# Performance work log

Hardware: AMD Instinct MI355X
Metric: run time of the kernel (lower is better)

## Reference

```python
import jax, jax.numpy as jnp
import numpy as np

N = 100000
E = 1600000
D = 64
BETA = 1.0


def setup_inputs() -> dict:
    key = jax.random.key(0)
    ks = jax.random.split(key, 6)
    x = jax.random.normal(ks[0], (N, D), dtype=jnp.float32)
    edge_index = jax.random.randint(ks[1], (2, E), 0, N, dtype=jnp.int64)
    s = 1.0 / np.sqrt(D)
    Wm = jax.random.uniform(ks[2], (D, D), jnp.float32, -s, s)
    bm = jax.random.uniform(ks[3], (D,), jnp.float32, -s, s)
    Wr = jax.random.uniform(ks[4], (D, D), jnp.float32, -s, s)
    br = jax.random.uniform(ks[5], (D,), jnp.float32, -s, s)
    return {"x": x, "edge_index": edge_index, "Wm": Wm, "bm": bm, "Wr": Wr, "br": br}


def reference(x, edge_index, Wm, bm, Wr, br):
    row, col = edge_index[0], edge_index[1]
    # gather source features and apply message linear: [E, D]
    messages = x[row] @ Wm + bm
    scores = BETA * messages.mean(axis=-1)  # [E]
    # edge softmax over incoming edges of each destination node (col)
    seg_max = jax.ops.segment_max(scores, col, num_segments=N)  # [N]
    ex = jnp.exp(scores - seg_max[col])  # [E]
    seg_sum = jax.ops.segment_sum(ex, col, num_segments=N)  # [N]
    weights = ex / seg_sum[col]  # [E]
    # weighted scatter-add back to destinations
    out = jax.ops.segment_sum(messages * weights[:, None], col, num_segments=N)
    return out + (x @ Wr + br)
```

## Files before the change

### kernel.cpp

```cpp
#include <hip/hip_runtime.h>
#include <math.h>

#define N_NODES 100000
#define DIM 64
#define N_EDGES 1600000

#define NBF 782
#define BK_NODES 128
#define CAP 3072

#define SC_CHUNK 8192
#define SC_BLOCKS ((N_EDGES + SC_CHUNK - 1) / SC_CHUNK)

#define GEMM_BLOCKS ((N_NODES / 16 + 15) / 16)
#define PH_BLOCKS (SC_BLOCKS + GEMM_BLOCKS)

typedef _Float16 half8 __attribute__((ext_vector_type(8)));
typedef _Float16 half4 __attribute__((ext_vector_type(4)));
typedef float f32x4 __attribute__((ext_vector_type(4)));

__global__ __launch_bounds__(1024) void k_phase(
        const float* __restrict__ x,
        const float* __restrict__ Wm, const float* __restrict__ bm,
        const float* __restrict__ Wr, const float* __restrict__ br,
        const int* __restrict__ row, const int* __restrict__ col,
        int* __restrict__ cursor, unsigned int* __restrict__ pairs,
        _Float16* __restrict__ Mh, float* __restrict__ es,
        float* __restrict__ out) {
    __shared__ int cnt[NBF];
    __shared__ int base_l[NBF];
    __shared__ int base_g[NBF];
    __shared__ int wsum[16];
    __shared__ unsigned int stage[SC_CHUNK];
    __shared__ unsigned short stage_bk[SC_CHUNK];

    const int t = threadIdx.x;
    const int lane = t & 63;
    const int wid = t >> 6;

    if (blockIdx.x < SC_BLOCKS) {
        const int start = blockIdx.x * SC_CHUNK;
        const int mEnd = min(N_EDGES, start + SC_CHUNK);

        for (int i = t; i < NBF; i += 1024) cnt[i] = 0;
        __syncthreads();

        int rr[8], cc[8], lr[8];
#pragma unroll
        for (int k = 0; k < 8; ++k) {
            const int idx = start + k * 1024 + t;
            if (idx < mEnd) {
                cc[k] = col[idx];
                rr[k] = row[idx];
                lr[k] = atomicAdd(&cnt[cc[k] >> 7], 1);
            }
        }
        __syncthreads();

        const int v = (t < NBF) ? cnt[t] : 0;
        int inc = v;
#pragma unroll
        for (int o = 1; o < 64; o <<= 1) {
            const int u = __shfl_up(inc, o, 64);
            if (lane >= o) inc += u;
        }
        if (lane == 63) wsum[wid] = inc;
        __syncthreads();
        if (wid == 0) {
            const int wv = (lane < 16) ? wsum[lane] : 0;
            int winc = wv;
#pragma unroll
            for (int o = 1; o < 16; o <<= 1) {
                const int u = __shfl_up(winc, o, 64);
                if (lane >= o) winc += u;
            }
            if (lane < 16) wsum[lane] = winc - wv;
        }
        __syncthreads();
        if (t < NBF) {
            base_l[t] = inc - v + wsum[wid];
            if (v > 0) base_g[t] = atomicAdd(&cursor[t], v);
        }
        __syncthreads();

#pragma unroll
        for (int k = 0; k < 8; ++k) {
            const int idx = start + k * 1024 + t;
            if (idx < mEnd) {
                const int bk = cc[k] >> 7;
                const int slot = base_l[bk] + lr[k];
                stage[slot] = ((unsigned int)rr[k] << 7) | (unsigned int)(cc[k] & 127);
                stage_bk[slot] = (unsigned short)bk;
            }
        }
        __syncthreads();

        const int m = mEnd - start;
        for (int i = t; i < m; i += 1024) {
            const int bk = stage_bk[i];
            const int gslot = base_g[bk] + (i - base_l[bk]);
            if (gslot < CAP) pairs[(size_t)bk * CAP + gslot] = stage[i];
        }
        return;
    }

    const int wave = (blockIdx.x - SC_BLOCKS) * 16 + wid;
    if (wave >= N_NODES / 16) return;
    const int quad = lane >> 4;
    const int l15 = lane & 15;
    const int row0 = wave * 16;

    half8 bfrag[8][2];
#pragma unroll
    for (int ct = 0; ct < 8; ++ct) {
        const float* W = (ct < 4) ? Wm : Wr;
        const int c = (ct & 3) * 16 + l15;
#pragma unroll
        for (int kc = 0; kc < 2; ++kc) {
            half8 f;
#pragma unroll
            for (int j = 0; j < 8; ++j)
                f[j] = (_Float16)W[(kc * 32 + quad * 8 + j) * DIM + c];
            bfrag[ct][kc] = f;
        }
    }

    half8 afrag[2];
#pragma unroll
    for (int kc = 0; kc < 2; ++kc) {
        const float* xp = x + (size_t)(row0 + l15) * DIM + kc * 32 + quad * 8;
        const float4 x0 = *(const float4*)xp;
        const float4 x1 = *(const float4*)(xp + 4);
        half8 f;
        f[0] = (_Float16)x0.x; f[1] = (_Float16)x0.y;
        f[2] = (_Float16)x0.z; f[3] = (_Float16)x0.w;
        f[4] = (_Float16)x1.x; f[5] = (_Float16)x1.y;
        f[6] = (_Float16)x1.z; f[7] = (_Float16)x1.w;
        afrag[kc] = f;
    }

    f32x4 acc[8];
#pragma unroll
    for (int ct = 0; ct < 8; ++ct) {
        f32x4 a = {0.f, 0.f, 0.f, 0.f};
        a = __builtin_amdgcn_mfma_f32_16x16x32_f16(afrag[0], bfrag[ct][0], a, 0, 0, 0);
        a = __builtin_amdgcn_mfma_f32_16x16x32_f16(afrag[1], bfrag[ct][1], a, 0, 0, 0);
        acc[ct] = a;
    }

    float rsum[4] = {0.f, 0.f, 0.f, 0.f};
#pragma unroll
    for (int ct = 0; ct < 8; ++ct) {
        const float bias = (ct < 4) ? bm[(ct & 3) * 16 + l15]
                                    : br[(ct & 3) * 16 + l15];
#pragma unroll
        for (int r = 0; r < 4; ++r) {
            const float v = acc[ct][r] + bias;
            const size_t idx = (size_t)(row0 + quad * 4 + r) * DIM + (ct & 3) * 16 + l15;
            if (ct < 4) {
                Mh[idx] = (_Float16)v;
                rsum[r] += v;
            } else {
                out[idx] = v;
            }
        }
    }
#pragma unroll
    for (int o = 1; o <= 8; o <<= 1) {
#pragma unroll
        for (int r = 0; r < 4; ++r) rsum[r] += __shfl_xor(rsum[r], o, 64);
    }
    if (l15 == 0) {
#pragma unroll
        for (int r = 0; r < 4; ++r)
            es[row0 + quad * 4 + r] = __expf(rsum[r] * (1.0f / DIM));
    }
}

__global__ __launch_bounds__(512) void k_bucket_gather(
        const unsigned int* __restrict__ pairs, const int* __restrict__ cursor,
        const float* __restrict__ es, const half4* __restrict__ Mh4,
        float4* __restrict__ out4) {
    __shared__ unsigned int sorted[CAP];
    __shared__ int cnt[BK_NODES];
    __shared__ int off[BK_NODES];
    const int b = blockIdx.x;
    const int t = threadIdx.x;
    const int m = min(cursor[b], CAP);
    const size_t base = (size_t)b * CAP;

    if (t < BK_NODES) cnt[t] = 0;
    __syncthreads();

    unsigned int pk[6];
    int rk[6];
#pragma unroll
    for (int k = 0; k < 6; ++k) {
        const int i = k * 512 + t;
        if (i < m) {
            pk[k] = pairs[base + i];
            rk[k] = atomicAdd(&cnt[pk[k] & 127u], 1);
        }
    }
    __syncthreads();

    int v = 0;
    if (t < BK_NODES) {
        v = cnt[t];
        off[t] = v;
    }
    __syncthreads();
    for (int o = 1; o < BK_NODES; o <<= 1) {
        int add = 0;
        if (t < BK_NODES && t >= o) add = off[t - o];
        __syncthreads();
        if (t < BK_NODES) off[t] += add;
        __syncthreads();
    }
    if (t < BK_NODES) off[t] -= v;
    __syncthreads();

#pragma unroll
    for (int k = 0; k < 6; ++k) {
        const int i = k * 512 + t;
        if (i < m) sorted[off[pk[k] & 127u] + rk[k]] = pk[k];
    }
    __syncthreads();

    const int g = t >> 4;
    const int gl = t & 15;
    for (int c = g; c < BK_NODES; c += 32) {
        const int node = b * BK_NODES + c;
        if (node >= N_NODES) break;
        const int s0i = off[c];
        const int len = cnt[c];
        if (len == 0) continue;

        float a0x = 0.f, a0y = 0.f, a0z = 0.f, a0w = 0.f, l0 = 0.f;
        float a1x = 0.f, a1y = 0.f, a1z = 0.f, a1w = 0.f, l1 = 0.f;
        int j = 0;
        for (; j + 1 < len; j += 2) {
            const int s0 = (int)(sorted[s0i + j] >> 7);
            const int s1 = (int)(sorted[s0i + j + 1] >> 7);
            const float w0 = es[s0];
            const float w1 = es[s1];
            const half4 m0 = Mh4[(size_t)s0 * 16 + gl];
            const half4 m1 = Mh4[(size_t)s1 * 16 + gl];
            l0 += w0; l1 += w1;
            a0x = fmaf(w0, (float)m0[0], a0x); a0y = fmaf(w0, (float)m0[1], a0y);
            a0z = fmaf(w0, (float)m0[2], a0z); a0w = fmaf(w0, (float)m0[3], a0w);
            a1x = fmaf(w1, (float)m1[0], a1x); a1y = fmaf(w1, (float)m1[1], a1y);
            a1z = fmaf(w1, (float)m1[2], a1z); a1w = fmaf(w1, (float)m1[3], a1w);
        }
        if (j < len) {
            const int s0 = (int)(sorted[s0i + j] >> 7);
            const float w0 = es[s0];
            const half4 m0 = Mh4[(size_t)s0 * 16 + gl];
            l0 += w0;
            a0x = fmaf(w0, (float)m0[0], a0x); a0y = fmaf(w0, (float)m0[1], a0y);
            a0z = fmaf(w0, (float)m0[2], a0z); a0w = fmaf(w0, (float)m0[3], a0w);
        }
        const float inv = 1.0f / (l0 + l1);
        float4 r = out4[(size_t)node * 16 + gl];
        r.x = fmaf(a0x + a1x, inv, r.x);
        r.y = fmaf(a0y + a1y, inv, r.y);
        r.z = fmaf(a0z + a1z, inv, r.z);
        r.w = fmaf(a0w + a1w, inv, r.w);
        out4[(size_t)node * 16 + gl] = r;
    }
}

extern "C" void kernel_launch(void* const* d_in, const int* in_sizes, int n_in,
                              void* d_out, int out_size, void* d_ws, size_t ws_size,
                              hipStream_t stream) {
    const float* x  = (const float*)d_in[0];
    const int*   ei = (const int*)d_in[1];
    const float* Wm = (const float*)d_in[2];
    const float* bm = (const float*)d_in[3];
    const float* Wr = (const float*)d_in[4];
    const float* br = (const float*)d_in[5];
    float* out = (float*)d_out;
    const int* row = ei;
    const int* col = ei + N_EDGES;

    char* ws = (char*)d_ws;
    _Float16* Mh    = (_Float16*)ws;     ws += (size_t)N_NODES * DIM * sizeof(_Float16);
    float* es       = (float*)ws;        ws += (size_t)N_NODES * sizeof(float);
    int* cursor     = (int*)ws;          ws += (size_t)1024 * sizeof(int);
    unsigned int* pairs = (unsigned int*)ws; ws += (size_t)NBF * CAP * sizeof(unsigned int);

    hipMemsetAsync(cursor, 0, NBF * sizeof(int), stream);

    k_phase<<<PH_BLOCKS, 1024, 0, stream>>>(x, Wm, bm, Wr, br, row, col,
                                            cursor, pairs, Mh, es, out);
    k_bucket_gather<<<NBF, 512, 0, stream>>>(pairs, cursor, es,
                                             (const half4*)Mh, (float4*)out);
}
```

Before: 157.3 us.

## Fuse scatter, GEMM and bucket gather into one persistent cooperative kernel

Replaces the memset plus two kernel launches with a single cooperative persistent kernel of 256 blocks. Work chunks are handed out through atomic tickets, and grid.sync separates the scatter/GEMM phase from the bucket-gather phase. The gather phase also moves from 512-thread to 1024-thread blocks. This removes launch and memset overhead and the inter-kernel gap, at the cost of grid-wide barriers, ticket atomics and fewer resident blocks for latency hiding in the gather.

```diff
diff --git a/kernel.cpp b/kernel.cpp
--- a/kernel.cpp
+++ b/kernel.cpp
@@ -1,5 +1,8 @@
 #include <hip/hip_runtime.h>
+#include <hip/hip_cooperative_groups.h>
 #include <math.h>
+
+namespace cg = cooperative_groups;
 
 #define N_NODES 100000
 #define DIM 64
@@ -11,262 +14,299 @@
 
 #define SC_CHUNK 8192
 #define SC_BLOCKS ((N_EDGES + SC_CHUNK - 1) / SC_CHUNK)
-
-#define GEMM_BLOCKS ((N_NODES / 16 + 15) / 16)
-#define PH_BLOCKS (SC_BLOCKS + GEMM_BLOCKS)
+#define GEMM_CHUNKS 391
+#define N_CHUNKS1 (SC_BLOCKS + GEMM_CHUNKS)
+
+#define GRID 256
+#define BLK 1024
 
 typedef _Float16 half8 __attribute__((ext_vector_type(8)));
 typedef _Float16 half4 __attribute__((ext_vector_type(4)));
 typedef float f32x4 __attribute__((ext_vector_type(4)));
 
-__global__ __launch_bounds__(1024) void k_phase(
+struct ScatterSh {
+    int cnt[NBF];
+    int base_l[NBF];
+    int base_g[NBF];
+    int wsum[16];
+    unsigned int stage[SC_CHUNK];
+    unsigned short stage_bk[SC_CHUNK];
+};
+struct BucketSh {
+    unsigned int sorted[CAP];
+    int cnt[BK_NODES];
+    int off[BK_NODES];
+};
+
+__global__ __launch_bounds__(BLK) void k_all(
         const float* __restrict__ x,
         const float* __restrict__ Wm, const float* __restrict__ bm,
         const float* __restrict__ Wr, const float* __restrict__ br,
         const int* __restrict__ row, const int* __restrict__ col,
-        int* __restrict__ cursor, unsigned int* __restrict__ pairs,
+        int* __restrict__ cursor, int* __restrict__ tickets,
+        unsigned int* __restrict__ pairs,
         _Float16* __restrict__ Mh, float* __restrict__ es,
         float* __restrict__ out) {
-    __shared__ int cnt[NBF];
-    __shared__ int base_l[NBF];
-    __shared__ int base_g[NBF];
-    __shared__ int wsum[16];
-    __shared__ unsigned int stage[SC_CHUNK];
-    __shared__ unsigned short stage_bk[SC_CHUNK];
+    __shared__ union { ScatterSh sc; BucketSh bk; } sh;
+    __shared__ int sb;
+    cg::grid_group grid = cg::this_grid();
 
     const int t = threadIdx.x;
     const int lane = t & 63;
     const int wid = t >> 6;
 
-    if (blockIdx.x < SC_BLOCKS) {
-        const int start = blockIdx.x * SC_CHUNK;
-        const int mEnd = min(N_EDGES, start + SC_CHUNK);
-
-        for (int i = t; i < NBF; i += 1024) cnt[i] = 0;
-        __syncthreads();
-
-        int rr[8], cc[8], lr[8];
-#pragma unroll
-        for (int k = 0; k < 8; ++k) {
-            const int idx = start + k * 1024 + t;
-            if (idx < mEnd) {
-                cc[k] = col[idx];
-                rr[k] = row[idx];
-                lr[k] = atomicAdd(&cnt[cc[k] >> 7], 1);
-            }
-        }
-        __syncthreads();
-
-        const int v = (t < NBF) ? cnt[t] : 0;
-        int inc = v;
-#pragma unroll
-        for (int o = 1; o < 64; o <<= 1) {
-            const int u = __shfl_up(inc, o, 64);
-            if (lane >= o) inc += u;
-        }
-        if (lane == 63) wsum[wid] = inc;
-        __syncthreads();
-        if (wid == 0) {
-            const int wv = (lane < 16) ? wsum[lane] : 0;
-            int winc = wv;
-#pragma unroll
-            for (int o = 1; o < 16; o <<= 1) {
-                const int u = __shfl_up(winc, o, 64);
-                if (lane >= o) winc += u;
-            }
-            if (lane < 16) wsum[lane] = winc - wv;
-        }
-        __syncthreads();
-        if (t < NBF) {
-            base_l[t] = inc - v + wsum[wid];
-            if (v > 0) base_g[t] = atomicAdd(&cursor[t], v);
-        }
-        __syncthreads();
-
-#pragma unroll
-        for (int k = 0; k < 8; ++k) {
-            const int idx = start + k * 1024 + t;
-            if (idx < mEnd) {
-                const int bk = cc[k] >> 7;
-                const int slot = base_l[bk] + lr[k];
-                stage[slot] = ((unsigned int)rr[k] << 7) | (unsigned int)(cc[k] & 127);
-                stage_bk[slot] = (unsigned short)bk;
-            }
-        }
-        __syncthreads();
-
-        const int m = mEnd - start;
-        for (int i = t; i < m; i += 1024) {
-            const int bk = stage_bk[i];
-            const int gslot = base_g[bk] + (i - base_l[bk]);
-            if (gslot < CAP) pairs[(size_t)bk * CAP + gslot] = stage[i];
-        }
-        return;
+    if (blockIdx.x == 0) {
+        if (t < NBF) cursor[t] = 0;
+        if (t >= 1022) tickets[t - 1022] = 0;
     }
-
-    const int wave = (blockIdx.x - SC_BLOCKS) * 16 + wid;
-    if (wave >= N_NODES / 16) return;
-    const int quad = lane >> 4;
-    const int l15 = lane & 15;
-    const int row0 = wave * 16;
-
-    half8 bfrag[8][2];
-#pragma unroll
-    for (int ct = 0; ct < 8; ++ct) {
-        const float* W = (ct < 4) ? Wm : Wr;
-        const int c = (ct & 3) * 16 + l15;
-#pragma unroll
-        for (int kc = 0; kc < 2; ++kc) {
-            half8 f;
-#pragma unroll
-            for (int j = 0; j < 8; ++j)
-                f[j] = (_Float16)W[(kc * 32 + quad * 8 + j) * DIM + c];
-            bfrag[ct][kc] = f;
+    grid.sync();
+
+    for (;;) {
+        if (t == 0) sb = atomicAdd(&tickets[0], 1);
+        __syncthreads();
+        const int cid = sb;
+        __syncthreads();
+        if (cid >= N_CHUNKS1) break;
+
+        if (cid < SC_BLOCKS) {
+            const int start = cid * SC_CHUNK;
+            const int mEnd = min(N_EDGES, start + SC_CHUNK);
+
+            for (int i = t; i < NBF; i += BLK) sh.sc.cnt[i] = 0;
+            __syncthreads();
+
+            int rr[8], cc[8], lr[8];
+#pragma unroll
+            for (int k = 0; k < 8; ++k) {
+                const int idx = start + k * BLK + t;
+                if (idx < mEnd) {
+                    cc[k] = col[idx];
+                    rr[k] = row[idx];
+                    lr[k] = atomicAdd(&sh.sc.cnt[cc[k] >> 7], 1);
+                }
+            }
+            __syncthreads();
+
+            const int v = (t < NBF) ? sh.sc.cnt[t] : 0;
+            int inc = v;
+#pragma unroll
+            for (int o = 1; o < 64; o <<= 1) {
+                const int u = __shfl_up(inc, o, 64);
+                if (lane >= o) inc += u;
+            }
+            if (lane == 63) sh.sc.wsum[wid] = inc;
+            __syncthreads();
+            if (wid == 0) {
+                const int wv = (lane < 16) ? sh.sc.wsum[lane] : 0;
+                int winc = wv;
+#pragma unroll
+                for (int o = 1; o < 16; o <<= 1) {
+                    const int u = __shfl_up(winc, o, 64);
+                    if (lane >= o) winc += u;
+                }
+                if (lane < 16) sh.sc.wsum[lane] = winc - wv;
+            }
+            __syncthreads();
+            if (t < NBF) {
+                sh.sc.base_l[t] = inc - v + sh.sc.wsum[wid];
+                if (v > 0) sh.sc.base_g[t] = atomicAdd(&cursor[t], v);
+            }
+            __syncthreads();
+
+#pragma unroll
+            for (int k = 0; k < 8; ++k) {
+                const int idx = start + k * BLK + t;
+                if (idx < mEnd) {
+                    const int bk = cc[k] >> 7;
+                    const int slot = sh.sc.base_l[bk] + lr[k];
+                    sh.sc.stage[slot] =
+                        ((unsigned int)rr[k] << 7) | (unsigned int)(cc[k] & 127);
+                    sh.sc.stage_bk[slot] = (unsigned short)bk;
+                }
+            }
+            __syncthreads();
+
+            const int m = mEnd - start;
+            for (int i = t; i < m; i += BLK) {
+                const int bk = sh.sc.stage_bk[i];
+                const int gslot = sh.sc.base_g[bk] + (i - sh.sc.base_l[bk]);
+                if (gslot < CAP) pairs[(size_t)bk * CAP + gslot] = sh.sc.stage[i];
+            }
+            __syncthreads();
+        } else {
+            const int wave = (cid - SC_BLOCKS) * 16 + wid;
+            if (wave < N_NODES / 16) {
+                const int quad = lane >> 4;
+                const int l15 = lane & 15;
+                const int row0 = wave * 16;
+
+                half8 bfrag[8][2];
+#pragma unroll
+                for (int ct = 0; ct < 8; ++ct) {
+                    const float* W = (ct < 4) ? Wm : Wr;
+                    const int c = (ct & 3) * 16 + l15;
+#pragma unroll
+                    for (int kc = 0; kc < 2; ++kc) {
+                        half8 f;
+#pragma unroll
+                        for (int j = 0; j < 8; ++j)
+                            f[j] = (_Float16)W[(kc * 32 + quad * 8 + j) * DIM + c];
+                        bfrag[ct][kc] = f;
+                    }
+                }
+
+                half8 afrag[2];
+#pragma unroll
+                for (int kc = 0; kc < 2; ++kc) {
+                    const float* xp = x + (size_t)(row0 + l15) * DIM + kc * 32 + quad * 8;
+                    const float4 x0 = *(const float4*)xp;
+                    const float4 x1 = *(const float4*)(xp + 4);
+                    half8 f;
+                    f[0] = (_Float16)x0.x; f[1] = (_Float16)x0.y;
+                    f[2] = (_Float16)x0.z; f[3] = (_Float16)x0.w;
+                    f[4] = (_Float16)x1.x; f[5] = (_Float16)x1.y;
+                    f[6] = (_Float16)x1.z; f[7] = (_Float16)x1.w;
+                    afrag[kc] = f;
+                }
+
+                f32x4 acc[8];
+#pragma unroll
+                for (int ct = 0; ct < 8; ++ct) {
+                    f32x4 a = {0.f, 0.f, 0.f, 0.f};
+                    a = __builtin_amdgcn_mfma_f32_16x16x32_f16(afrag[0], bfrag[ct][0], a, 0, 0, 0);
+                    a = __builtin_amdgcn_mfma_f32_16x16x32_f16(afrag[1], bfrag[ct][1], a, 0, 0, 0);
+                    acc[ct] = a;
+                }
+
+                float rsum[4] = {0.f, 0.f, 0.f, 0.f};
+#pragma unroll
+                for (int ct = 0; ct < 8; ++ct) {
+                    const float bias = (ct < 4) ? bm[(ct & 3) * 16 + l15]
+                                                : br[(ct & 3) * 16 + l15];
+#pragma unroll
+                    for (int r = 0; r < 4; ++r) {
+                        const float vv = acc[ct][r] + bias;
+                        const size_t idx =
+                            (size_t)(row0 + quad * 4 + r) * DIM + (ct & 3) * 16 + l15;
+                        if (ct < 4) {
+                            Mh[idx] = (_Float16)vv;
+                            rsum[r] += vv;
+                        } else {
+                            out[idx] = vv;
+                        }
+                    }
+                }
+#pragma unroll
+                for (int o = 1; o <= 8; o <<= 1) {
+#pragma unroll
+                    for (int r = 0; r < 4; ++r) rsum[r] += __shfl_xor(rsum[r], o, 64);
+                }
+                if (l15 == 0) {
+#pragma unroll
+                    for (int r = 0; r < 4; ++r)
+                        es[row0 + quad * 4 + r] = __expf(rsum[r] * (1.0f / DIM));
+                }
+            }
+            __syncthreads();
         }
     }
 
-    half8 afrag[2];
-#pragma unroll
-    for (int kc = 0; kc < 2; ++kc) {
-        const float* xp = x + (size_t)(row0 + l15) * DIM + kc * 32 + quad * 8;
-        const float4 x0 = *(const float4*)xp;
-        const float4 x1 = *(const float4*)(xp + 4);
-        half8 f;
-        f[0] = (_Float16)x0.x; f[1] = (_Float16)x0.y;
-        f[2] = (_Float16)x0.z; f[3] = (_Float16)x0.w;
-        f[4] = (_Float16)x1.x; f[5] = (_Float16)x1.y;
-        f[6] = (_Float16)x1.z; f[7] = (_Float16)x1.w;
-        afrag[kc] = f;
-    }
-
-    f32x4 acc[8];
-#pragma unroll
-    for (int ct = 0; ct < 8; ++ct) {
-        f32x4 a = {0.f, 0.f, 0.f, 0.f};
-        a = __builtin_amdgcn_mfma_f32_16x16x32_f16(afrag[0], bfrag[ct][0], a, 0, 0, 0);
-        a = __builtin_amdgcn_mfma_f32_16x16x32_f16(afrag[1], bfrag[ct][1], a, 0, 0, 0);
-        acc[ct] = a;
-    }
-
-    float rsum[4] = {0.f, 0.f, 0.f, 0.f};
-#pragma unroll
-    for (int ct = 0; ct < 8; ++ct) {
-        const float bias = (ct < 4) ? bm[(ct & 3) * 16 + l15]
-                                    : br[(ct & 3) * 16 + l15];
-#pragma unroll
-        for (int r = 0; r < 4; ++r) {
-            const float v = acc[ct][r] + bias;
-            const size_t idx = (size_t)(row0 + quad * 4 + r) * DIM + (ct & 3) * 16 + l15;
-            if (ct < 4) {
-                Mh[idx] = (_Float16)v;
-                rsum[r] += v;
-            } else {
-                out[idx] = v;
-            }
-        }
-    }
-#pragma unroll
-    for (int o = 1; o <= 8; o <<= 1) {
-#pragma unroll
-        for (int r = 0; r < 4; ++r) rsum[r] += __shfl_xor(rsum[r], o, 64);
-    }
-    if (l15 == 0) {
-#pragma unroll
-        for (int r = 0; r < 4; ++r)
-            es[row0 + quad * 4 + r] = __expf(rsum[r] * (1.0f / DIM));
-    }
-}
-
-__global__ __launch_bounds__(512) void k_bucket_gather(
-        const unsigned int* __restrict__ pairs, const int* __restrict__ cursor,
-        const float* __restrict__ es, const half4* __restrict__ Mh4,
-        float4* __restrict__ out4) {
-    __shared__ unsigned int sorted[CAP];
-    __shared__ int cnt[BK_NODES];
-    __shared__ int off[BK_NODES];
-    const int b = blockIdx.x;
-    const int t = threadIdx.x;
-    const int m = min(cursor[b], CAP);
-    const size_t base = (size_t)b * CAP;
-
-    if (t < BK_NODES) cnt[t] = 0;
-    __syncthreads();
-
-    unsigned int pk[6];
-    int rk[6];
-#pragma unroll
-    for (int k = 0; k < 6; ++k) {
-        const int i = k * 512 + t;
-        if (i < m) {
-            pk[k] = pairs[base + i];
-            rk[k] = atomicAdd(&cnt[pk[k] & 127u], 1);
-        }
-    }
-    __syncthreads();
-
-    int v = 0;
-    if (t < BK_NODES) {
-        v = cnt[t];
-        off[t] = v;
-    }
-    __syncthreads();
-    for (int o = 1; o < BK_NODES; o <<= 1) {
-        int add = 0;
-        if (t < BK_NODES && t >= o) add = off[t - o];
-        __syncthreads();
-        if (t < BK_NODES) off[t] += add;
-        __syncthreads();
-    }
-    if (t < BK_NODES) off[t] -= v;
-    __syncthreads();
-
-#pragma unroll
-    for (int k = 0; k < 6; ++k) {
-        const int i = k * 512 + t;
-        if (i < m) sorted[off[pk[k] & 127u] + rk[k]] = pk[k];
-    }
-    __syncthreads();
-
-    const int g = t >> 4;
-    const int gl = t & 15;
-    for (int c = g; c < BK_NODES; c += 32) {
-        const int node = b * BK_NODES + c;
-        if (node >= N_NODES) break;
-        const int s0i = off[c];
-        const int len = cnt[c];
-        if (len == 0) continue;
-
-        float a0x = 0.f, a0y = 0.f, a0z = 0.f, a0w = 0.f, l0 = 0.f;
-        float a1x = 0.f, a1y = 0.f, a1z = 0.f, a1w = 0.f, l1 = 0.f;
-        int j = 0;
-        for (; j + 1 < len; j += 2) {
-            const int s0 = (int)(sorted[s0i + j] >> 7);
-            const int s1 = (int)(sorted[s0i + j + 1] >> 7);
-            const float w0 = es[s0];
-            const float w1 = es[s1];
-            const half4 m0 = Mh4[(size_t)s0 * 16 + gl];
-            const half4 m1 = Mh4[(size_t)s1 * 16 + gl];
-            l0 += w0; l1 += w1;
-            a0x = fmaf(w0, (float)m0[0], a0x); a0y = fmaf(w0, (float)m0[1], a0y);
-            a0z = fmaf(w0, (float)m0[2], a0z); a0w = fmaf(w0, (float)m0[3], a0w);
-            a1x = fmaf(w1, (float)m1[0], a1x); a1y = fmaf(w1, (float)m1[1], a1y);
-            a1z = fmaf(w1, (float)m1[2], a1z); a1w = fmaf(w1, (float)m1[3], a1w);
-        }
-        if (j < len) {
-            const int s0 = (int)(sorted[s0i + j] >> 7);
-            const float w0 = es[s0];
-            const half4 m0 = Mh4[(size_t)s0 * 16 + gl];
-            l0 += w0;
-            a0x = fmaf(w0, (float)m0[0], a0x); a0y = fmaf(w0, (float)m0[1], a0y);
-            a0z = fmaf(w0, (float)m0[2], a0z); a0w = fmaf(w0, (float)m0[3], a0w);
-        }
-        const float inv = 1.0f / (l0 + l1);
-        float4 r = out4[(size_t)node * 16 + gl];
-        r.x = fmaf(a0x + a1x, inv, r.x);
-        r.y = fmaf(a0y + a1y, inv, r.y);
-        r.z = fmaf(a0z + a1z, inv, r.z);
-        r.w = fmaf(a0w + a1w, inv, r.w);
-        out4[(size_t)node * 16 + gl] = r;
+    grid.sync();
+
+    for (;;) {
+        if (t == 0) sb = atomicAdd(&tickets[1], 1);
+        __syncthreads();
+        const int b = sb;
+        __syncthreads();
+        if (b >= NBF) break;
+
+        const int m = min(cursor[b], CAP);
+        const size_t base = (size_t)b * CAP;
+
+        if (t < BK_NODES) sh.bk.cnt[t] = 0;
+        __syncthreads();
+
+        unsigned int pk[3];
+        int rk[3];
+#pragma unroll
+        for (int k = 0; k < 3; ++k) {
+            const int i = k * BLK + t;
+            if (i < m) {
+                pk[k] = pairs[base + i];
+                rk[k] = atomicAdd(&sh.bk.cnt[pk[k] & 127u], 1);
+            }
+        }
+        __syncthreads();
+
+        int v = 0;
+        if (t < BK_NODES) {
+            v = sh.bk.cnt[t];
+            sh.bk.off[t] = v;
+        }
+        __syncthreads();
+        for (int o = 1; o < BK_NODES; o <<= 1) {
+            int add = 0;
+            if (t < BK_NODES && t >= o) add = sh.bk.off[t - o];
+            __syncthreads();
+            if (t < BK_NODES) sh.bk.off[t] += add;
+            __syncthreads();
+        }
+        if (t < BK_NODES) sh.bk.off[t] -= v;
+        __syncthreads();
+
+#pragma unroll
+        for (int k = 0; k < 3; ++k) {
+            const int i = k * BLK + t;
+            if (i < m) sh.bk.sorted[sh.bk.off[pk[k] & 127u] + rk[k]] = pk[k];
+        }
+        __syncthreads();
+
+        const int g = t >> 4;
+        const int gl = t & 15;
+        const half4* __restrict__ Mh4 = (const half4*)Mh;
+        float4* __restrict__ out4 = (float4*)out;
+#pragma unroll
+        for (int cc = 0; cc < 2; ++cc) {
+            const int c = g + cc * 64;
+            const int node = b * BK_NODES + c;
+            if (node >= N_NODES) continue;
+            const int s0i = sh.bk.off[c];
+            const int len = sh.bk.cnt[c];
+            if (len == 0) continue;
+
+            float a0x = 0.f, a0y = 0.f, a0z = 0.f, a0w = 0.f, l0 = 0.f;
+            float a1x = 0.f, a1y = 0.f, a1z = 0.f, a1w = 0.f, l1 = 0.f;
+            int j = 0;
+            for (; j + 1 < len; j += 2) {
+                const int s0 = (int)(sh.bk.sorted[s0i + j] >> 7);
+                const int s1 = (int)(sh.bk.sorted[s0i + j + 1] >> 7);
+                const float w0 = es[s0];
+                const float w1 = es[s1];
+                const half4 m0 = Mh4[(size_t)s0 * 16 + gl];
+                const half4 m1 = Mh4[(size_t)s1 * 16 + gl];
+                l0 += w0; l1 += w1;
+                a0x = fmaf(w0, (float)m0[0], a0x); a0y = fmaf(w0, (float)m0[1], a0y);
+                a0z = fmaf(w0, (float)m0[2], a0z); a0w = fmaf(w0, (float)m0[3], a0w);
+                a1x = fmaf(w1, (float)m1[0], a1x); a1y = fmaf(w1, (float)m1[1], a1y);
+                a1z = fmaf(w1, (float)m1[2], a1z); a1w = fmaf(w1, (float)m1[3], a1w);
+            }
+            if (j < len) {
+                const int s0 = (int)(sh.bk.sorted[s0i + j] >> 7);
+                const float w0 = es[s0];
+                const half4 m0 = Mh4[(size_t)s0 * 16 + gl];
+                l0 += w0;
+                a0x = fmaf(w0, (float)m0[0], a0x); a0y = fmaf(w0, (float)m0[1], a0y);
+                a0z = fmaf(w0, (float)m0[2], a0z); a0w = fmaf(w0, (float)m0[3], a0w);
+            }
+            const float inv = 1.0f / (l0 + l1);
+            float4 r = out4[(size_t)node * 16 + gl];
+            r.x = fmaf(a0x + a1x, inv, r.x);
+            r.y = fmaf(a0y + a1y, inv, r.y);
+            r.z = fmaf(a0z + a1z, inv, r.z);
+            r.w = fmaf(a0w + a1w, inv, r.w);
+            out4[(size_t)node * 16 + gl] = r;
+        }
+        __syncthreads();
     }
 }
 
@@ -287,12 +327,11 @@
     _Float16* Mh    = (_Float16*)ws;     ws += (size_t)N_NODES * DIM * sizeof(_Float16);
     float* es       = (float*)ws;        ws += (size_t)N_NODES * sizeof(float);
     int* cursor     = (int*)ws;          ws += (size_t)1024 * sizeof(int);
+    int* tickets    = (int*)ws;          ws += (size_t)64 * sizeof(int);
     unsigned int* pairs = (unsigned int*)ws; ws += (size_t)NBF * CAP * sizeof(unsigned int);
 
-    hipMemsetAsync(cursor, 0, NBF * sizeof(int), stream);
-
-    k_phase<<<PH_BLOCKS, 1024, 0, stream>>>(x, Wm, bm, Wr, br, row, col,
-                                            cursor, pairs, Mh, es, out);
-    k_bucket_gather<<<NBF, 512, 0, stream>>>(pairs, cursor, es,
-                                             (const half4*)Mh, (float4*)out);
+    void* args[] = {(void*)&x, (void*)&Wm, (void*)&bm, (void*)&Wr, (void*)&br,
+                    (void*)&row, (void*)&col, (void*)&cursor, (void*)&tickets,
+                    (void*)&pairs, (void*)&Mh, (void*)&es, (void*)&out};
+    hipLaunchCooperativeKernel((void*)k_all, dim3(GRID), dim3(BLK), args, 0, stream);
 }
```

New measurement: 283.5 us. +80.2%, slower.
